# Kernel optimization log

Hardware: AMD Instinct MI355X
Metric: run time of the kernel (lower is better)

## Reference

```python
import jax, jax.numpy as jnp
import numpy as np

DIM = 1024
HEADS = 16
HEAD_DIM = DIM // HEADS
SCALE = HEAD_DIM ** -0.5


def setup_inputs() -> dict:
    key = jax.random.key(0)
    ks = jax.random.split(key, 6)
    B, N = 2, 2048
    s = DIM ** -0.5
    return {
        "x": jax.random.normal(ks[0], (B, N, DIM), dtype=jnp.float32),
        "Wq": jax.random.normal(ks[1], (DIM, DIM), dtype=jnp.float32) * s,
        "Wk": jax.random.normal(ks[2], (DIM, DIM), dtype=jnp.float32) * s,
        "Wv": jax.random.normal(ks[3], (DIM, DIM), dtype=jnp.float32) * s,
        "Wo": jax.random.normal(ks[4], (DIM, DIM), dtype=jnp.float32) * s,
        "bo": jnp.zeros((DIM,), dtype=jnp.float32),
    }


def reference(x, Wq, Wk, Wv, Wo, bo):
    B, N, D = x.shape
    # Linear projections (torch Linear: y = x @ W.T)
    q = x @ Wq.T
    k = x @ Wk.T
    v = x @ Wv.T
    # [B, H, N, hd]
    q = q.reshape(B, N, HEADS, HEAD_DIM).transpose(0, 2, 1, 3)
    k = k.reshape(B, N, HEADS, HEAD_DIM).transpose(0, 2, 1, 3)
    v = v.reshape(B, N, HEADS, HEAD_DIM).transpose(0, 2, 1, 3)
    scores = jnp.einsum('bhid,bhjd->bhij', q, k) * SCALE
    probs = jax.nn.softmax(scores, axis=-1)
    out = jnp.einsum('bhij,bhjd->bhid', probs, v)
    out = out.transpose(0, 2, 1, 3).reshape(B, N, D)
    return out @ Wo.T + bo
```

## Files before the change

kernel.cpp:

```cpp
#include <hip/hip_runtime.h>

#define DIM    1024
#define HEADS  16
#define HD     64
#define BATCH  2
#define SEQ    2048
#define C2     0.18033688011112042f

typedef __attribute__((ext_vector_type(8))) short           short8;
typedef __attribute__((ext_vector_type(4))) short           short4v;
typedef __attribute__((ext_vector_type(4))) float           f4;
typedef __attribute__((ext_vector_type(4))) unsigned short  u16x4;
typedef __attribute__((ext_vector_type(4))) unsigned int    u32x4;
typedef __attribute__((ext_vector_type(2))) unsigned int    u32x2;

typedef __attribute__((address_space(3))) unsigned int       as3_u32;
typedef const __attribute__((address_space(1))) unsigned int as1_u32;

__device__ __forceinline__ unsigned short f2bf(float f) {
    unsigned int u = __builtin_bit_cast(unsigned int, f);
    u = (u + 0x7fffu + ((u >> 16) & 1u)) >> 16;
    return (unsigned short)u;
}
__device__ __forceinline__ unsigned int pk_bf16(float a, float b) {
    return (unsigned int)f2bf(a) | ((unsigned int)f2bf(b) << 16);
}

#if __has_builtin(__builtin_amdgcn_exp2f)
#define EXP2(x) __builtin_amdgcn_exp2f(x)
#else
#define EXP2(x) exp2f(x)
#endif

__device__ __forceinline__ void gl2lds16(const unsigned short* g, unsigned short* l) {
    __builtin_amdgcn_global_load_lds((as1_u32*)g, (as3_u32*)l, 16, 0, 0);
}

__global__ __launch_bounds__(256) void k_cast_all(
    const float* __restrict__ x,  const float* __restrict__ wq,
    const float* __restrict__ wk, const float* __restrict__ wv,
    const float* __restrict__ wo, unsigned short* __restrict__ dst)
{
    const int i = blockIdx.x * 256 + threadIdx.x;
    const float* src;
    int off;
    if (i < (1 << 20))            { src = x;  off = 0; }
    else if (i < (5 << 18))       { src = wq; off = 1 << 20; }
    else if (i < (6 << 18))       { src = wk; off = 5 << 18; }
    else if (i < (7 << 18))       { src = wv; off = 6 << 18; }
    else                          { src = wo; off = 7 << 18; }
    f4 v = ((const f4*)src)[i - off];
    u16x4 o;
    o[0] = f2bf(v[0]); o[1] = f2bf(v[1]); o[2] = f2bf(v[2]); o[3] = f2bf(v[3]);
    ((u16x4*)dst)[i] = o;
}

__global__ __launch_bounds__(256) void gemm_qkv(
    const unsigned short* __restrict__ A,
    const unsigned short* __restrict__ Wq,
    const unsigned short* __restrict__ Wk,
    const unsigned short* __restrict__ Wv,
    unsigned short* __restrict__ Qo,
    unsigned short* __restrict__ Ko,
    unsigned short* __restrict__ Vo)
{
    __shared__ __align__(16) unsigned short Xs[128 * 32];
    __shared__ __align__(16) unsigned short Ws[128 * 32];
    const int L   = blockIdx.x;
    const int xcd = L & 7;
    const int idx = L >> 3;
    const int col = idx >> 2;
    const int sb  = (xcd * 4 + (idx & 3)) * 128;
    const int wsel = col >> 3;
    const int fb   = (col & 7) * 128;
    const unsigned short* W = (wsel == 0) ? Wq : ((wsel == 1) ? Wk : Wv);

    const int tid  = threadIdx.x;
    const int wave = tid >> 6, lane = tid & 63;
    const int quad = lane >> 4, l16 = lane & 15;
    const int wm = (wave & 1) << 6, wn = (wave >> 1) << 6;

    const unsigned short* aLDS = (wsel < 2) ? Ws : Xs;
    const unsigned short* bLDS = (wsel < 2) ? Xs : Ws;

    f4 acc[4][4] = {};

    for (int k0 = 0; k0 < DIM; k0 += 32) {
        __syncthreads();
        #pragma unroll
        for (int i = 0; i < 2; i++) {
            const int c = tid + (i << 8);
            const int row = c >> 2, koff = (c & 3) << 3;
            gl2lds16(&A[(size_t)(sb + row) * DIM + k0 + koff], &Xs[(size_t)((i << 8) + (wave << 6)) * 8]);
            gl2lds16(&W[(size_t)(fb + row) * DIM + k0 + koff], &Ws[(size_t)((i << 8) + (wave << 6)) * 8]);
        }
        __syncthreads();
        short8 afr[4], bfr[4];
        #pragma unroll
        for (int i = 0; i < 4; i++)
            afr[i] = *(const short8*)(&aLDS[(wm + i * 16 + l16) * 32 + quad * 8]);
        #pragma unroll
        for (int j = 0; j < 4; j++)
            bfr[j] = *(const short8*)(&bLDS[(wn + j * 16 + l16) * 32 + quad * 8]);
        #pragma unroll
        for (int i = 0; i < 4; i++)
            #pragma unroll
            for (int j = 0; j < 4; j++)
                acc[i][j] = __builtin_amdgcn_mfma_f32_16x16x32_bf16(afr[i], bfr[j], acc[i][j], 0, 0, 0);
    }

    if (wsel < 2) {
        unsigned short* out = (wsel == 0) ? Qo : Ko;
        const float sc = (wsel == 0) ? C2 : 1.0f;
        #pragma unroll
        for (int j = 0; j < 4; j++) {
            const int ms = sb + wn + j * 16 + l16;
            const int b = ms >> 11, ns = ms & (SEQ - 1);
            #pragma unroll
            for (int i = 0; i < 4; i++) {
                const int feat = fb + wm + i * 16 + quad * 4;
                const int h = feat >> 6, d = feat & (HD - 1);
                u32x2 pw;
                pw[0] = pk_bf16(acc[i][j][0] * sc, acc[i][j][1] * sc);
                pw[1] = pk_bf16(acc[i][j][2] * sc, acc[i][j][3] * sc);
                *(u32x2*)(&out[((size_t)(b * HEADS + h) * SEQ + ns) * HD + d]) = pw;
            }
        }
    } else {
        #pragma unroll
        for (int j = 0; j < 4; j++) {
            const int feat = fb + wn + j * 16 + l16;
            const int h = feat >> 6, d = feat & (HD - 1);
            #pragma unroll
            for (int i = 0; i < 4; i++) {
                const int ms = sb + wm + i * 16 + quad * 4;
                const int b = ms >> 11, ns = ms & (SEQ - 1);
                u32x2 pw;
                pw[0] = pk_bf16(acc[i][j][0], acc[i][j][1]);
                pw[1] = pk_bf16(acc[i][j][2], acc[i][j][3]);
                *(u32x2*)(&Vo[((size_t)(b * HEADS + h) * HD + d) * SEQ + ns]) = pw;
            }
        }
    }
}

__global__ __launch_bounds__(256) void attn_fwd(
    const unsigned short* __restrict__ Qg,
    const unsigned short* __restrict__ Kg,
    const unsigned short* __restrict__ VTg,
    unsigned short* __restrict__ AOb)
{
    __shared__ __align__(16) unsigned short QsP[128 * 72];
    __shared__ __align__(16) unsigned short Ks [64 * 72];
    __shared__ __align__(16) unsigned short VsT[64 * 72];

    const int L   = blockIdx.x;
    const int xcd = L & 7;
    const int idx = L >> 3;
    const int bh  = xcd * 4 + (idx >> 4);
    const int q0  = (idx & 15) << 7;

    const unsigned short* Qb  = Qg  + (size_t)bh * SEQ * HD;
    const unsigned short* Kb  = Kg  + (size_t)bh * SEQ * HD;
    const unsigned short* VTb = VTg + (size_t)bh * HD * SEQ;

    const int tid  = threadIdx.x;
    const int wave = tid >> 6, lane = tid & 63;
    const int quad = lane >> 4, l16 = lane & 15;
    const int qw   = wave << 5;
    const int r8   = tid >> 3;
    const int g8   = (tid & 7) * 8;

    #pragma unroll
    for (int p = 0; p < 4; p++) {
        const int row = r8 + p * 32;
        *(u32x4*)(&QsP[row * 72 + g8]) = *(const u32x4*)(&Qb[(size_t)(q0 + row) * HD + g8]);
    }
    #pragma unroll
    for (int p = 0; p < 2; p++) {
        const int row = r8 + p * 32;
        *(u32x4*)(&Ks [row * 72 + g8]) = *(const u32x4*)(&Kb [(size_t)row * HD + g8]);
        *(u32x4*)(&VsT[row * 72 + g8]) = *(const u32x4*)(&VTb[(size_t)row * SEQ + g8]);
    }
    __syncthreads();

    short8 qf[2][2];
    #pragma unroll
    for (int nf = 0; nf < 2; nf++)
        #pragma unroll
        for (int ks = 0; ks < 2; ks++)
            qf[nf][ks] = *(const short8*)(&QsP[(qw + nf * 16 + l16) * 72 + ks * 32 + quad * 8]);

    f4 lsum[2] = {};
    f4 Oacc[4][2] = {};

    for (int kt = 0; kt < SEQ / 64; kt++) {
        u32x4 kpre[2], vpre[2];
        if (kt < SEQ / 64 - 1) {
            #pragma unroll
            for (int p = 0; p < 2; p++) {
                const int row = r8 + p * 32;
                kpre[p] = *(const u32x4*)(&Kb [(size_t)((kt + 1) * 64 + row) * HD + g8]);
                vpre[p] = *(const u32x4*)(&VTb[(size_t)row * SEQ + (kt + 1) * 64 + g8]);
            }
        }

        f4 sacc[4][2] = {};
        #pragma unroll
        for (int ks = 0; ks < 2; ks++) {
            short8 kfr[4];
            #pragma unroll
            for (int mf = 0; mf < 4; mf++)
                kfr[mf] = *(const short8*)(&Ks[(mf * 16 + l16) * 72 + ks * 32 + quad * 8]);
            #pragma unroll
            for (int mf = 0; mf < 4; mf++)
                #pragma unroll
                for (int nf = 0; nf < 2; nf++)
                    sacc[mf][nf] = __builtin_amdgcn_mfma_f32_16x16x32_bf16(kfr[mf], qf[nf][ks], sacc[mf][nf], 0, 0, 0);
        }

#if __has_builtin(__builtin_amdgcn_mfma_f32_16x16x16bf16_1k)
        short4v pb[2][4];
        #pragma unroll
        for (int nf = 0; nf < 2; nf++) {
            #pragma unroll
            for (int mf = 0; mf < 4; mf++) {
                f4 pv;
                #pragma unroll
                for (int r = 0; r < 4; r++)
                    pv[r] = EXP2(sacc[mf][nf][r]);
                lsum[nf] += pv;
                short4v pk;
                #pragma unroll
                for (int r = 0; r < 4; r++)
                    pk[r] = (short)f2bf(pv[r]);
                pb[nf][mf] = pk;
            }
        }
        #pragma unroll
        for (int ks16 = 0; ks16 < 4; ks16++) {
            short4v vfr[4];
            #pragma unroll
            for (int mf = 0; mf < 4; mf++)
                vfr[mf] = *(const short4v*)(&VsT[(mf * 16 + l16) * 72 + ks16 * 16 + quad * 4]);
            #pragma unroll
            for (int mf = 0; mf < 4; mf++)
                #pragma unroll
                for (int nf = 0; nf < 2; nf++)
                    Oacc[mf][nf] = __builtin_amdgcn_mfma_f32_16x16x16bf16_1k(vfr[mf], pb[nf][ks16], Oacc[mf][nf], 0, 0, 0);
        }
#else
        #pragma unroll
        for (int nf = 0; nf < 2; nf++) {
            #pragma unroll
            for (int mf = 0; mf < 4; mf++) {
                f4 pv;
                #pragma unroll
                for (int r = 0; r < 4; r++)
                    pv[r] = EXP2(sacc[mf][nf][r]);
                lsum[nf] += pv;
                u32x2 pw;
                pw[0] = pk_bf16(pv[0], pv[1]);
                pw[1] = pk_bf16(pv[2], pv[3]);
                *(u32x2*)(&QsP[(qw + nf * 16 + l16) * 72 + mf * 16 + quad * 4]) = pw;
            }
        }
        #pragma unroll
        for (int ks = 0; ks < 2; ks++) {
            short8 vfr[4], pf[2];
            #pragma unroll
            for (int mf = 0; mf < 4; mf++)
                vfr[mf] = *(const short8*)(&VsT[(mf * 16 + l16) * 72 + ks * 32 + quad * 8]);
            #pragma unroll
            for (int nf = 0; nf < 2; nf++)
                pf[nf] = *(const short8*)(&QsP[(qw + nf * 16 + l16) * 72 + ks * 32 + quad * 8]);
            #pragma unroll
            for (int mf = 0; mf < 4; mf++)
                #pragma unroll
                for (int nf = 0; nf < 2; nf++)
                    Oacc[mf][nf] = __builtin_amdgcn_mfma_f32_16x16x32_bf16(vfr[mf], pf[nf], Oacc[mf][nf], 0, 0, 0);
        }
#endif

        __syncthreads();
        if (kt < SEQ / 64 - 1) {
            #pragma unroll
            for (int p = 0; p < 2; p++) {
                const int row = r8 + p * 32;
                *(u32x4*)(&Ks [row * 72 + g8]) = kpre[p];
                *(u32x4*)(&VsT[row * 72 + g8]) = vpre[p];
            }
        }
        __syncthreads();
    }

    const int b = bh >> 4, h = bh & (HEADS - 1);
    #pragma unroll
    for (int nf = 0; nf < 2; nf++) {
        float l = lsum[nf][0] + lsum[nf][1] + lsum[nf][2] + lsum[nf][3];
        l += __shfl_xor(l, 16);
        l += __shfl_xor(l, 32);
        const float inv = 1.0f / l;
        const int qg = q0 + qw + nf * 16 + l16;
        #pragma unroll
        for (int mf = 0; mf < 4; mf++) {
            u32x2 o;
            o[0] = pk_bf16(Oacc[mf][nf][0] * inv, Oacc[mf][nf][1] * inv);
            o[1] = pk_bf16(Oacc[mf][nf][2] * inv, Oacc[mf][nf][3] * inv);
            *(u32x2*)(&AOb[(size_t)(b * SEQ + qg) * DIM + h * HD + mf * 16 + quad * 4]) = o;
        }
    }
}

__global__ __launch_bounds__(256) void gemm_out(
    const unsigned short* __restrict__ AO,
    const unsigned short* __restrict__ W,
    float* __restrict__ out,
    const float* __restrict__ bias)
{
    __shared__ __align__(16) unsigned short As[64 * 32];
    __shared__ __align__(16) unsigned short Bs[128 * 32];
    const int L   = blockIdx.x;
    const int xcd = L & 7;
    const int idx = L >> 3;
    const int n0  = (xcd * 4 + (idx >> 4)) * 128;
    const int m0  = (idx & 15) * 64;

    const int tid  = threadIdx.x;
    const int wave = tid >> 6, lane = tid & 63;
    const int quad = lane >> 4, l16 = lane & 15;
    const int wm = (wave & 1) << 5, wn = (wave >> 1) << 6;

    f4 acc[2][4] = {};

    for (int k0 = 0; k0 < DIM; k0 += 32) {
        __syncthreads();
        gl2lds16(&W[(size_t)(m0 + (tid >> 2)) * DIM + k0 + ((tid & 3) << 3)],
                 &As[(size_t)(wave << 6) * 8]);
        #pragma unroll
        for (int i = 0; i < 2; i++) {
            const int c = tid + (i << 8);
            gl2lds16(&AO[(size_t)(n0 + (c >> 2)) * DIM + k0 + ((c & 3) << 3)],
                     &Bs[(size_t)((i << 8) + (wave << 6)) * 8]);
        }
        __syncthreads();
        short8 afr[2], bfr[4];
        #pragma unroll
        for (int i = 0; i < 2; i++)
            afr[i] = *(const short8*)(&As[(wm + i * 16 + l16) * 32 + quad * 8]);
        #pragma unroll
        for (int j = 0; j < 4; j++)
            bfr[j] = *(const short8*)(&Bs[(wn + j * 16 + l16) * 32 + quad * 8]);
        #pragma unroll
        for (int i = 0; i < 2; i++)
            #pragma unroll
            for (int j = 0; j < 4; j++)
                acc[i][j] = __builtin_amdgcn_mfma_f32_16x16x32_bf16(afr[i], bfr[j], acc[i][j], 0, 0, 0);
    }

    #pragma unroll
    for (int i = 0; i < 2; i++) {
        const int feat = m0 + wm + i * 16 + quad * 4;
        const f4 bv = *(const f4*)(&bias[feat]);
        #pragma unroll
        for (int j = 0; j < 4; j++) {
            const int ns = n0 + wn + j * 16 + l16;
            *(f4*)(&out[(size_t)ns * DIM + feat]) = acc[i][j] + bv;
        }
    }
}

extern "C" void kernel_launch(void* const* d_in, const int* in_sizes, int n_in,
                              void* d_out, int out_size, void* d_ws, size_t ws_size,
                              hipStream_t stream) {
    (void)in_sizes; (void)n_in; (void)out_size; (void)ws_size;
    const float* x  = (const float*)d_in[0];
    const float* Wq = (const float*)d_in[1];
    const float* Wk = (const float*)d_in[2];
    const float* Wv = (const float*)d_in[3];
    const float* Wo = (const float*)d_in[4];
    const float* bo = (const float*)d_in[5];

    unsigned short* wsu = (unsigned short*)d_ws;
    unsigned short* xb  = wsu;
    unsigned short* Wqb = wsu + (4u  << 20);
    unsigned short* Wkb = wsu + (5u  << 20);
    unsigned short* Wvb = wsu + (6u  << 20);
    unsigned short* Wob = wsu + (7u  << 20);
    unsigned short* Qb  = wsu + (8u  << 20);
    unsigned short* Kb  = wsu + (12u << 20);
    unsigned short* VTb = wsu + (16u << 20);
    unsigned short* AOb = wsu + (20u << 20);

    k_cast_all<<<8192, 256, 0, stream>>>(x, Wq, Wk, Wv, Wo, wsu);

    gemm_qkv<<<768, 256, 0, stream>>>(xb, Wqb, Wkb, Wvb, Qb, Kb, VTb);

    attn_fwd<<<512, 256, 0, stream>>>(Qb, Kb, VTb, AOb);

    gemm_out<<<512, 256, 0, stream>>>(AOb, Wob, (float*)d_out, bo);
}
```

Before: 193.8 us.

## Load attention K/V fragments directly from global into registers, drop LDS staging

The attention kernel no longer stages Q, K and V^T tiles through shared memory with two barriers per iteration. Each wave now loads its MFMA fragments straight from global memory into registers, double-buffering K fragments and prefetching V per step, and the launch bounds request two blocks per CU. This removes the LDS round-trips and __syncthreads, but every wave now fetches the full K/V tile independently, relying on L1/L2 instead of sharing through LDS, and it raises register pressure.

```diff
diff --git a/kernel.cpp b/kernel.cpp
--- a/kernel.cpp
+++ b/kernel.cpp
@@ -144,16 +144,15 @@
     }
 }
 
-__global__ __launch_bounds__(256) void attn_fwd(
+__global__ __launch_bounds__(256, 2) void attn_fwd(
     const unsigned short* __restrict__ Qg,
     const unsigned short* __restrict__ Kg,
     const unsigned short* __restrict__ VTg,
     unsigned short* __restrict__ AOb)
 {
-    __shared__ __align__(16) unsigned short QsP[128 * 72];
-    __shared__ __align__(16) unsigned short Ks [64 * 72];
-    __shared__ __align__(16) unsigned short VsT[64 * 72];
-
+#if !__has_builtin(__builtin_amdgcn_mfma_f32_16x16x16bf16_1k)
+    __shared__ __align__(16) unsigned short Ps[128 * 72];
+#endif
     const int L   = blockIdx.x;
     const int xcd = L & 7;
     const int idx = L >> 3;
@@ -168,56 +167,49 @@
     const int wave = tid >> 6, lane = tid & 63;
     const int quad = lane >> 4, l16 = lane & 15;
     const int qw   = wave << 5;
-    const int r8   = tid >> 3;
-    const int g8   = (tid & 7) * 8;
-
-    #pragma unroll
-    for (int p = 0; p < 4; p++) {
-        const int row = r8 + p * 32;
-        *(u32x4*)(&QsP[row * 72 + g8]) = *(const u32x4*)(&Qb[(size_t)(q0 + row) * HD + g8]);
-    }
-    #pragma unroll
-    for (int p = 0; p < 2; p++) {
-        const int row = r8 + p * 32;
-        *(u32x4*)(&Ks [row * 72 + g8]) = *(const u32x4*)(&Kb [(size_t)row * HD + g8]);
-        *(u32x4*)(&VsT[row * 72 + g8]) = *(const u32x4*)(&VTb[(size_t)row * SEQ + g8]);
-    }
-    __syncthreads();
 
     short8 qf[2][2];
     #pragma unroll
     for (int nf = 0; nf < 2; nf++)
         #pragma unroll
         for (int ks = 0; ks < 2; ks++)
-            qf[nf][ks] = *(const short8*)(&QsP[(qw + nf * 16 + l16) * 72 + ks * 32 + quad * 8]);
+            qf[nf][ks] = *(const short8*)(&Qb[(size_t)(q0 + qw + nf * 16 + l16) * HD + ks * 32 + quad * 8]);
+
+    const unsigned short* kp = Kb  + (size_t)l16 * HD  + quad * 8;
+    const unsigned short* vp = VTb + (size_t)l16 * SEQ + quad * 4;
 
     f4 lsum[2] = {};
     f4 Oacc[4][2] = {};
 
-    for (int kt = 0; kt < SEQ / 64; kt++) {
-        u32x4 kpre[2], vpre[2];
-        if (kt < SEQ / 64 - 1) {
-            #pragma unroll
-            for (int p = 0; p < 2; p++) {
-                const int row = r8 + p * 32;
-                kpre[p] = *(const u32x4*)(&Kb [(size_t)((kt + 1) * 64 + row) * HD + g8]);
-                vpre[p] = *(const u32x4*)(&VTb[(size_t)row * SEQ + (kt + 1) * 64 + g8]);
-            }
-        }
-
+    short8  kfA[4][2], kfB[4][2];
+    short4v vf[4][4];
+
+    auto LOADK = [&](short8 (&kf)[4][2], int kt) {
+        const unsigned short* p = kp + (size_t)kt * 64 * HD;
+        #pragma unroll
+        for (int mf = 0; mf < 4; mf++)
+            #pragma unroll
+            for (int ks = 0; ks < 2; ks++)
+                kf[mf][ks] = *(const short8*)(p + mf * 16 * HD + ks * 32);
+    };
+    auto LOADV = [&](short4v (&v)[4][4], int kt) {
+        const unsigned short* p = vp + kt * 64;
+        #pragma unroll
+        for (int ks16 = 0; ks16 < 4; ks16++)
+            #pragma unroll
+            for (int mf = 0; mf < 4; mf++)
+                v[ks16][mf] = *(const short4v*)(p + (size_t)mf * 16 * SEQ + ks16 * 16);
+    };
+
+    auto STEP = [&](const short8 (&kf)[4][2], const short4v (&v)[4][4]) {
         f4 sacc[4][2] = {};
         #pragma unroll
-        for (int ks = 0; ks < 2; ks++) {
-            short8 kfr[4];
+        for (int ks = 0; ks < 2; ks++)
             #pragma unroll
             for (int mf = 0; mf < 4; mf++)
-                kfr[mf] = *(const short8*)(&Ks[(mf * 16 + l16) * 72 + ks * 32 + quad * 8]);
-            #pragma unroll
-            for (int mf = 0; mf < 4; mf++)
                 #pragma unroll
                 for (int nf = 0; nf < 2; nf++)
-                    sacc[mf][nf] = __builtin_amdgcn_mfma_f32_16x16x32_bf16(kfr[mf], qf[nf][ks], sacc[mf][nf], 0, 0, 0);
-        }
+                    sacc[mf][nf] = __builtin_amdgcn_mfma_f32_16x16x32_bf16(kf[mf][ks], qf[nf][ks], sacc[mf][nf], 0, 0, 0);
 
 #if __has_builtin(__builtin_amdgcn_mfma_f32_16x16x16bf16_1k)
         short4v pb[2][4];
@@ -238,17 +230,12 @@
             }
         }
         #pragma unroll
-        for (int ks16 = 0; ks16 < 4; ks16++) {
-            short4v vfr[4];
+        for (int ks16 = 0; ks16 < 4; ks16++)
             #pragma unroll
             for (int mf = 0; mf < 4; mf++)
-                vfr[mf] = *(const short4v*)(&VsT[(mf * 16 + l16) * 72 + ks16 * 16 + quad * 4]);
-            #pragma unroll
-            for (int mf = 0; mf < 4; mf++)
                 #pragma unroll
                 for (int nf = 0; nf < 2; nf++)
-                    Oacc[mf][nf] = __builtin_amdgcn_mfma_f32_16x16x16bf16_1k(vfr[mf], pb[nf][ks16], Oacc[mf][nf], 0, 0, 0);
-        }
+                    Oacc[mf][nf] = __builtin_amdgcn_mfma_f32_16x16x16bf16_1k(v[ks16][mf], pb[nf][ks16], Oacc[mf][nf], 0, 0, 0);
 #else
         #pragma unroll
         for (int nf = 0; nf < 2; nf++) {
@@ -262,36 +249,36 @@
                 u32x2 pw;
                 pw[0] = pk_bf16(pv[0], pv[1]);
                 pw[1] = pk_bf16(pv[2], pv[3]);
-                *(u32x2*)(&QsP[(qw + nf * 16 + l16) * 72 + mf * 16 + quad * 4]) = pw;
+                *(u32x2*)(&Ps[(qw + nf * 16 + l16) * 72 + mf * 16 + quad * 4]) = pw;
             }
         }
         #pragma unroll
         for (int ks = 0; ks < 2; ks++) {
-            short8 vfr[4], pf[2];
-            #pragma unroll
-            for (int mf = 0; mf < 4; mf++)
-                vfr[mf] = *(const short8*)(&VsT[(mf * 16 + l16) * 72 + ks * 32 + quad * 8]);
+            short8 pf[2];
             #pragma unroll
             for (int nf = 0; nf < 2; nf++)
-                pf[nf] = *(const short8*)(&QsP[(qw + nf * 16 + l16) * 72 + ks * 32 + quad * 8]);
-            #pragma unroll
-            for (int mf = 0; mf < 4; mf++)
+                pf[nf] = *(const short8*)(&Ps[(qw + nf * 16 + l16) * 72 + ks * 32 + quad * 8]);
+            #pragma unroll
+            for (int mf = 0; mf < 4; mf++) {
+                short8 v8;
+                #pragma unroll
+                for (int e = 0; e < 4; e++) { v8[e] = v[ks * 2][mf][e]; v8[e + 4] = v[ks * 2 + 1][mf][e]; }
                 #pragma unroll
                 for (int nf = 0; nf < 2; nf++)
-                    Oacc[mf][nf] = __builtin_amdgcn_mfma_f32_16x16x32_bf16(vfr[mf], pf[nf], Oacc[mf][nf], 0, 0, 0);
+                    Oacc[mf][nf] = __builtin_amdgcn_mfma_f32_16x16x32_bf16(v8, pf[nf], Oacc[mf][nf], 0, 0, 0);
+            }
         }
 #endif
-
-        __syncthreads();
-        if (kt < SEQ / 64 - 1) {
-            #pragma unroll
-            for (int p = 0; p < 2; p++) {
-                const int row = r8 + p * 32;
-                *(u32x4*)(&Ks [row * 72 + g8]) = kpre[p];
-                *(u32x4*)(&VsT[row * 72 + g8]) = vpre[p];
-            }
-        }
-        __syncthreads();
+    };
+
+    LOADK(kfA, 0);
+    for (int kt = 0; kt < SEQ / 64; kt += 2) {
+        LOADV(vf, kt);
+        LOADK(kfB, kt + 1);
+        STEP(kfA, vf);
+        LOADV(vf, kt + 1);
+        if (kt + 2 < SEQ / 64) LOADK(kfA, kt + 2);
+        STEP(kfB, vf);
     }
 
     const int b = bh >> 4, h = bh & (HEADS - 1);
```

Measured after the change: 309.1 us. 1.59x slower.

## Double-buffer K/V tiles in attention, load Q directly, use hardware bf16 pack

Applied to the files above, without the earlier changes.

Moves the attention kernel's K and V shared-memory tiles to two buffers, so the next tile is written into the alternate buffer and each iteration needs one barrier instead of two. Q fragments are now loaded straight from global memory into registers instead of being staged through shared memory, which frees the Q shared-memory array. It also adds a launch-bounds occupancy hint, raises wave priority around the MFMA blocks, and uses the v_cvt_pk_bf16_f32 instruction to pack probabilities into bf16. The single barrier is only safe if no wave can still be reading the buffer that is being overwritten. Hardware bf16 rounding may also differ slightly from the software conversion.

```diff
diff --git a/kernel.cpp b/kernel.cpp
--- a/kernel.cpp
+++ b/kernel.cpp
@@ -24,6 +24,11 @@
 }
 __device__ __forceinline__ unsigned int pk_bf16(float a, float b) {
     return (unsigned int)f2bf(a) | ((unsigned int)f2bf(b) << 16);
+}
+__device__ __forceinline__ unsigned int pk_bf16_hw(float a, float b) {
+    unsigned int r;
+    asm("v_cvt_pk_bf16_f32 %0, %1, %2" : "=v"(r) : "v"(a), "v"(b));
+    return r;
 }
 
 #if __has_builtin(__builtin_amdgcn_exp2f)
@@ -144,15 +149,17 @@
     }
 }
 
-__global__ __launch_bounds__(256) void attn_fwd(
+__global__ __launch_bounds__(256, 2) void attn_fwd(
     const unsigned short* __restrict__ Qg,
     const unsigned short* __restrict__ Kg,
     const unsigned short* __restrict__ VTg,
     unsigned short* __restrict__ AOb)
 {
-    __shared__ __align__(16) unsigned short QsP[128 * 72];
-    __shared__ __align__(16) unsigned short Ks [64 * 72];
-    __shared__ __align__(16) unsigned short VsT[64 * 72];
+    __shared__ __align__(16) unsigned short Ks [2][64 * 72];
+    __shared__ __align__(16) unsigned short VsT[2][64 * 72];
+#if !__has_builtin(__builtin_amdgcn_mfma_f32_16x16x16bf16_1k)
+    __shared__ __align__(16) unsigned short Ps[128 * 72];
+#endif
 
     const int L   = blockIdx.x;
     const int xcd = L & 7;
@@ -171,28 +178,24 @@
     const int r8   = tid >> 3;
     const int g8   = (tid & 7) * 8;
 
+    short8 qf[2][2];
     #pragma unroll
-    for (int p = 0; p < 4; p++) {
-        const int row = r8 + p * 32;
-        *(u32x4*)(&QsP[row * 72 + g8]) = *(const u32x4*)(&Qb[(size_t)(q0 + row) * HD + g8]);
-    }
+    for (int nf = 0; nf < 2; nf++)
+        #pragma unroll
+        for (int ks = 0; ks < 2; ks++)
+            qf[nf][ks] = *(const short8*)(&Qb[(size_t)(q0 + qw + nf * 16 + l16) * HD + ks * 32 + quad * 8]);
+
     #pragma unroll
     for (int p = 0; p < 2; p++) {
         const int row = r8 + p * 32;
-        *(u32x4*)(&Ks [row * 72 + g8]) = *(const u32x4*)(&Kb [(size_t)row * HD + g8]);
-        *(u32x4*)(&VsT[row * 72 + g8]) = *(const u32x4*)(&VTb[(size_t)row * SEQ + g8]);
+        *(u32x4*)(&Ks [0][row * 72 + g8]) = *(const u32x4*)(&Kb [(size_t)row * HD + g8]);
+        *(u32x4*)(&VsT[0][row * 72 + g8]) = *(const u32x4*)(&VTb[(size_t)row * SEQ + g8]);
     }
     __syncthreads();
-
-    short8 qf[2][2];
-    #pragma unroll
-    for (int nf = 0; nf < 2; nf++)
-        #pragma unroll
-        for (int ks = 0; ks < 2; ks++)
-            qf[nf][ks] = *(const short8*)(&QsP[(qw + nf * 16 + l16) * 72 + ks * 32 + quad * 8]);
 
     f4 lsum[2] = {};
     f4 Oacc[4][2] = {};
+    int cur = 0;
 
     for (int kt = 0; kt < SEQ / 64; kt++) {
         u32x4 kpre[2], vpre[2];
@@ -204,20 +207,24 @@
                 vpre[p] = *(const u32x4*)(&VTb[(size_t)row * SEQ + (kt + 1) * 64 + g8]);
             }
         }
+        const unsigned short* ksb = &Ks [cur][0];
+        const unsigned short* vsb = &VsT[cur][0];
 
         f4 sacc[4][2] = {};
+        __builtin_amdgcn_s_setprio(1);
         #pragma unroll
         for (int ks = 0; ks < 2; ks++) {
             short8 kfr[4];
             #pragma unroll
             for (int mf = 0; mf < 4; mf++)
-                kfr[mf] = *(const short8*)(&Ks[(mf * 16 + l16) * 72 + ks * 32 + quad * 8]);
+                kfr[mf] = *(const short8*)(&ksb[(mf * 16 + l16) * 72 + ks * 32 + quad * 8]);
             #pragma unroll
             for (int mf = 0; mf < 4; mf++)
                 #pragma unroll
                 for (int nf = 0; nf < 2; nf++)
                     sacc[mf][nf] = __builtin_amdgcn_mfma_f32_16x16x32_bf16(kfr[mf], qf[nf][ks], sacc[mf][nf], 0, 0, 0);
         }
+        __builtin_amdgcn_s_setprio(0);
 
 #if __has_builtin(__builtin_amdgcn_mfma_f32_16x16x16bf16_1k)
         short4v pb[2][4];
@@ -230,25 +237,26 @@
                 for (int r = 0; r < 4; r++)
                     pv[r] = EXP2(sacc[mf][nf][r]);
                 lsum[nf] += pv;
-                short4v pk;
-                #pragma unroll
-                for (int r = 0; r < 4; r++)
-                    pk[r] = (short)f2bf(pv[r]);
-                pb[nf][mf] = pk;
-            }
-        }
+                u32x2 pw;
+                pw[0] = pk_bf16_hw(pv[0], pv[1]);
+                pw[1] = pk_bf16_hw(pv[2], pv[3]);
+                pb[nf][mf] = __builtin_bit_cast(short4v, pw);
+            }
+        }
+        __builtin_amdgcn_s_setprio(1);
         #pragma unroll
         for (int ks16 = 0; ks16 < 4; ks16++) {
             short4v vfr[4];
             #pragma unroll
             for (int mf = 0; mf < 4; mf++)
-                vfr[mf] = *(const short4v*)(&VsT[(mf * 16 + l16) * 72 + ks16 * 16 + quad * 4]);
+                vfr[mf] = *(const short4v*)(&vsb[(mf * 16 + l16) * 72 + ks16 * 16 + quad * 4]);
             #pragma unroll
             for (int mf = 0; mf < 4; mf++)
                 #pragma unroll
                 for (int nf = 0; nf < 2; nf++)
                     Oacc[mf][nf] = __builtin_amdgcn_mfma_f32_16x16x16bf16_1k(vfr[mf], pb[nf][ks16], Oacc[mf][nf], 0, 0, 0);
         }
+        __builtin_amdgcn_s_setprio(0);
 #else
         #pragma unroll
         for (int nf = 0; nf < 2; nf++) {
@@ -262,7 +270,7 @@
                 u32x2 pw;
                 pw[0] = pk_bf16(pv[0], pv[1]);
                 pw[1] = pk_bf16(pv[2], pv[3]);
-                *(u32x2*)(&QsP[(qw + nf * 16 + l16) * 72 + mf * 16 + quad * 4]) = pw;
+                *(u32x2*)(&Ps[(qw + nf * 16 + l16) * 72 + mf * 16 + quad * 4]) = pw;
             }
         }
         #pragma unroll
@@ -270,10 +278,10 @@
             short8 vfr[4], pf[2];
             #pragma unroll
             for (int mf = 0; mf < 4; mf++)
-                vfr[mf] = *(const short8*)(&VsT[(mf * 16 + l16) * 72 + ks * 32 + quad * 8]);
+                vfr[mf] = *(const short8*)(&vsb[(mf * 16 + l16) * 72 + ks * 32 + quad * 8]);
             #pragma unroll
             for (int nf = 0; nf < 2; nf++)
-                pf[nf] = *(const short8*)(&QsP[(qw + nf * 16 + l16) * 72 + ks * 32 + quad * 8]);
+                pf[nf] = *(const short8*)(&Ps[(qw + nf * 16 + l16) * 72 + ks * 32 + quad * 8]);
             #pragma unroll
             for (int mf = 0; mf < 4; mf++)
                 #pragma unroll
@@ -282,16 +290,16 @@
         }
 #endif
 
-        __syncthreads();
         if (kt < SEQ / 64 - 1) {
             #pragma unroll
             for (int p = 0; p < 2; p++) {
                 const int row = r8 + p * 32;
-                *(u32x4*)(&Ks [row * 72 + g8]) = kpre[p];
-                *(u32x4*)(&VsT[row * 72 + g8]) = vpre[p];
-            }
-        }
-        __syncthreads();
+                *(u32x4*)(&Ks [cur ^ 1][row * 72 + g8]) = kpre[p];
+                *(u32x4*)(&VsT[cur ^ 1][row * 72 + g8]) = vpre[p];
+            }
+            __syncthreads();
+        }
+        cur ^= 1;
     }
 
     const int b = bh >> 4, h = bh & (HEADS - 1);
```

New measurement: 184.7 us. 4.7% less time.
